# Kernel tuning notes

Hardware: AMD Instinct MI355X
Metric: run time of the kernel (lower is better)

The kernel has to match this reference:

```python
import jax, jax.numpy as jnp
import numpy as np

N = 100000   # total nodes in batched graph
E = 320000   # total edges
B = 128      # number of graphs in batch
D_IN = 128
H = 256
OUT = 10
L = 4        # num_layers - 1 conv layers
EPS = 1e-6


def setup_inputs() -> dict:
    key = jax.random.key(0)
    ks = jax.random.split(key, 8)
    h = jax.random.normal(ks[0], (N, D_IN), dtype=jnp.float32)
    src = jax.random.randint(ks[1], (E,), 0, N)
    dst = jax.random.randint(ks[2], (E,), 0, N)
    batch_ids = jnp.sort(jax.random.randint(ks[3], (N,), 0, B))
    s = 0.05
    W_first = jax.random.normal(ks[4], (D_IN, H), dtype=jnp.float32) * s
    b_first = jnp.zeros((H,), jnp.float32)
    W_rest = jax.random.normal(ks[5], (L - 1, H, H), dtype=jnp.float32) * s
    b_rest = jnp.zeros((L - 1, H), jnp.float32)
    gamma = jnp.ones((L, H), jnp.float32)
    beta = jnp.zeros((L, H), jnp.float32)
    mean_scale = jnp.ones((L, H), jnp.float32)
    W_pred = jax.random.normal(ks[6], (H, OUT), dtype=jnp.float32) * s
    b_pred = jnp.zeros((OUT,), jnp.float32)
    return dict(h=h, src=src, dst=dst, batch_ids=batch_ids,
                W_first=W_first, b_first=b_first, W_rest=W_rest, b_rest=b_rest,
                gamma=gamma, beta=beta, mean_scale=mean_scale,
                W_pred=W_pred, b_pred=b_pred)


def _graph_conv(h, W, b, src, dst, dinv_src, dinv_dst):
    # DGL GraphConv, norm='both': D_dst^{-1/2} A D_src^{-1/2} h W + b
    x = h * dinv_src[:, None]
    m = jax.ops.segment_sum(x[src], dst, num_segments=N)
    m = m * dinv_dst[:, None]
    return m @ W + b


def _graph_norm(h, gamma, beta, ms, batch_ids, counts):
    # GraphNorm: per-graph mean (scaled by learnable mean_scale) and std
    mean = jax.ops.segment_sum(h, batch_ids, num_segments=B) / counts[:, None]
    sub = h - mean[batch_ids] * ms
    var = jax.ops.segment_sum(sub * sub, batch_ids, num_segments=B) / counts[:, None]
    inv_std = jax.lax.rsqrt(var + EPS)
    return gamma * sub * inv_std[batch_ids] + beta


def reference(h, src, dst, batch_ids, W_first, b_first, W_rest, b_rest,
              gamma, beta, mean_scale, W_pred, b_pred):
    ones_e = jnp.ones((E,), h.dtype)
    deg_out = jnp.maximum(jax.ops.segment_sum(ones_e, src, num_segments=N), 1.0)
    deg_in = jnp.maximum(jax.ops.segment_sum(ones_e, dst, num_segments=N), 1.0)
    dinv_src = jax.lax.rsqrt(deg_out)
    dinv_dst = jax.lax.rsqrt(deg_in)
    counts = jnp.maximum(
        jax.ops.segment_sum(jnp.ones((N,), h.dtype), batch_ids, num_segments=B), 1.0)

    for i in range(L):
        x = h
        if i == 0:
            h = _graph_conv(h, W_first, b_first, src, dst, dinv_src, dinv_dst)
        else:
            h = _graph_conv(h, W_rest[i - 1], b_rest[i - 1], src, dst, dinv_src, dinv_dst)
        h = _graph_norm(h, gamma[i], beta[i], mean_scale[i], batch_ids, counts)
        if i != 0:
            h = jax.nn.relu(h) + x
        else:
            h = jax.nn.relu(h)

    pooled = jax.ops.segment_sum(h, batch_ids, num_segments=B)  # [B, H]
    # dropout is identity at eval
    return pooled @ W_pred + b_pred
```

## Files before the change

kernel.cpp:

```cpp
#include <hip/hip_runtime.h>

#define N_NODES 100000
#define N_PAD   100096
#define N_EDGES 320000
#define NB      128
#define DIN     128
#define H       256
#define OUT_DIM 10
#define EPSV    1e-6f
#define SCAN_B  256
#define PSLICES 32

typedef unsigned short bf16_t;
typedef __attribute__((ext_vector_type(8))) short bf16x8;
typedef __attribute__((ext_vector_type(4))) float f32x4;

__device__ __forceinline__ float bf2f(bf16_t u) {
    union { unsigned int i; float f; } x;
    x.i = ((unsigned int)u) << 16;
    return x.f;
}
__device__ __forceinline__ bf16_t f2bf(float f) {
    union { float f; unsigned int i; } x;
    x.f = f;
    unsigned int r = x.i + 0x7fffu + ((x.i >> 16) & 1u);
    return (bf16_t)(r >> 16);
}

__global__ void k_edge_deg(const int* __restrict__ src, const int* __restrict__ dst,
                           int* deg_out, int* deg_in) {
    int e = blockIdx.x * blockDim.x + threadIdx.x;
    if (e < N_EDGES) {
        atomicAdd(&deg_out[src[e]], 1);
        atomicAdd(&deg_in[dst[e]], 1);
    }
}

__global__ void k_dinv(const int* __restrict__ deg_out, const int* __restrict__ deg_in,
                       float* dinv_src, float* dinv_dst) {
    int n = blockIdx.x * blockDim.x + threadIdx.x;
    if (n < N_NODES) {
        dinv_src[n] = rsqrtf((float)max(deg_out[n], 1));
        dinv_dst[n] = rsqrtf((float)max(deg_in[n], 1));
    }
}

__global__ void k_gstart(const int* __restrict__ bid, int* __restrict__ gstart,
                         float* __restrict__ countsf) {
    int b = threadIdx.x;
    if (b <= NB) {
        int lo = 0, hi = N_NODES;
        while (lo < hi) {
            int mid = (lo + hi) >> 1;
            if (bid[mid] < b) lo = mid + 1; else hi = mid;
        }
        gstart[b] = lo;
    }
    __syncthreads();
    if (b < NB) countsf[b] = (float)max(gstart[b + 1] - gstart[b], 1);
}

__global__ void k_scan1(const int* __restrict__ deg, int* incl, int* bsums) {
    __shared__ int s[SCAN_B];
    int i = blockIdx.x * SCAN_B + threadIdx.x;
    int v = (i < N_NODES) ? deg[i] : 0;
    s[threadIdx.x] = v;
    __syncthreads();
    for (int d = 1; d < SCAN_B; d <<= 1) {
        int t = (threadIdx.x >= d) ? s[threadIdx.x - d] : 0;
        __syncthreads();
        s[threadIdx.x] += t;
        __syncthreads();
    }
    if (i < N_NODES) incl[i] = s[threadIdx.x];
    if (threadIdx.x == SCAN_B - 1) bsums[blockIdx.x] = s[threadIdx.x];
}

__global__ void k_scan2(const int* __restrict__ bsums, int* boffs, int nb) {
    __shared__ int s[512];
    int t = threadIdx.x;
    int v = (t < nb) ? bsums[t] : 0;
    s[t] = v;
    __syncthreads();
    for (int d = 1; d < 512; d <<= 1) {
        int x = (t >= d) ? s[t - d] : 0;
        __syncthreads();
        s[t] += x;
        __syncthreads();
    }
    if (t < nb) boffs[t] = s[t] - v;
}

__global__ void k_scan3(const int* __restrict__ deg, const int* __restrict__ incl,
                        const int* __restrict__ boffs, int* row_start, int* cursor) {
    int i = blockIdx.x * blockDim.x + threadIdx.x;
    if (i < N_NODES) {
        int ex = incl[i] - deg[i] + boffs[i / SCAN_B];
        row_start[i] = ex;
        cursor[i]    = ex;
    }
    if (i == 0) row_start[N_NODES] = N_EDGES;
}

__global__ void k_scatter(const int* __restrict__ src, const int* __restrict__ dst,
                          int* cursor, int* csr_src) {
    int e = blockIdx.x * blockDim.x + threadIdx.x;
    if (e < N_EDGES) {
        int slot = atomicAdd(&cursor[dst[e]], 1);
        csr_src[slot] = src[e];
    }
}

__global__ void k_wt_first(const float* __restrict__ W, bf16_t* __restrict__ Wt) {
    int idx = blockIdx.x * 256 + threadIdx.x;
    if (idx >= H * DIN) return;
    int c = idx / DIN, k = idx % DIN;
    Wt[idx] = f2bf(W[k * H + c]);
}
__global__ void k_wt_rest(const float* __restrict__ W, bf16_t* __restrict__ Wt) {
    int idx = blockIdx.x * 256 + threadIdx.x;
    if (idx >= 3 * H * H) return;
    int l = idx / (H * H);
    int rem = idx % (H * H);
    int c = rem / H, k = rem % H;
    Wt[idx] = f2bf(W[(size_t)l * H * H + k * H + c]);
}

__global__ void k_prescale(const float* __restrict__ h, const float* __restrict__ dinv_s,
                           bf16_t* __restrict__ hs) {
    int idx = blockIdx.x * blockDim.x + threadIdx.x;
    if (idx >= N_NODES * (DIN / 4)) return;
    int n = idx >> 5;
    float w = dinv_s[n];
    float4 v = reinterpret_cast<const float4*>(h)[idx];
    ushort4 o;
    o.x = f2bf(v.x * w); o.y = f2bf(v.y * w);
    o.z = f2bf(v.z * w); o.w = f2bf(v.w * w);
    reinterpret_cast<ushort4*>(hs)[idx] = o;
}

template <int NC, bool PS>
__global__ void k_agg(const bf16_t* __restrict__ hx, const float* __restrict__ dinv_s,
                      const float* __restrict__ dinv_d, const int* __restrict__ row_start,
                      const int* __restrict__ csr_src, bf16_t* __restrict__ m) {
    constexpr int VEC = NC / 64;
    int gid  = blockIdx.x * blockDim.x + threadIdx.x;
    int v    = gid >> 6;
    int lane = gid & 63;
    if (v >= N_NODES) return;
    float acc[VEC] = {};
    int s0 = row_start[v], s1 = row_start[v + 1];

    auto body = [&](int ei) {
        int si = csr_src[ei];
        float wv = 1.f;
        if constexpr (!PS) wv = dinv_s[si];
        if constexpr (VEC == 4) {
            ushort4 r = *reinterpret_cast<const ushort4*>(hx + (size_t)si * NC + lane * 4);
            acc[0] += bf2f(r.x) * wv; acc[1] += bf2f(r.y) * wv;
            acc[2] += bf2f(r.z) * wv; acc[3] += bf2f(r.w) * wv;
        } else {
            ushort2 r = *reinterpret_cast<const ushort2*>(hx + (size_t)si * NC + lane * 2);
            acc[0] += bf2f(r.x) * wv; acc[1] += bf2f(r.y) * wv;
        }
    };

    int e = s0;
    for (; e + 3 < s1; e += 4) { body(e); body(e + 1); body(e + 2); body(e + 3); }
    for (; e < s1; ++e) body(e);

    float wd = dinv_d[v];
    if constexpr (VEC == 4) {
        ushort4 o;
        o.x = f2bf(acc[0] * wd); o.y = f2bf(acc[1] * wd);
        o.z = f2bf(acc[2] * wd); o.w = f2bf(acc[3] * wd);
        *reinterpret_cast<ushort4*>(m + (size_t)v * NC + lane * 4) = o;
    } else {
        ushort2 o; o.x = f2bf(acc[0] * wd); o.y = f2bf(acc[1] * wd);
        *reinterpret_cast<ushort2*>(m + (size_t)v * NC + lane * 2) = o;
    }
}

template <int K>
__global__ __launch_bounds__(256) void k_gemm_mfma(const bf16_t* __restrict__ A,
                                                   const bf16_t* __restrict__ Wt,
                                                   const float* __restrict__ bias,
                                                   bf16_t* __restrict__ C) {
    __shared__ bf16_t lds_raw[64 * (H + 8)];
    constexpr int LKA = K + 8;
    bf16_t (*aT)[LKA] = reinterpret_cast<bf16_t (*)[LKA]>(lds_raw);
    bf16_t (*cT)[H + 8] = reinterpret_cast<bf16_t (*)[H + 8]>(lds_raw);

    const int tid  = threadIdx.x;
    const int wave = tid >> 6;
    const int lane = tid & 63;
    const int row0 = blockIdx.x * 64;
    const int col0 = wave * 64;
    const int lr = lane & 15;
    const int lg = lane >> 4;

    {
        const bf16_t* Ag = A + (size_t)row0 * K;
        constexpr int CHUNKS = 64 * K / 8;
        #pragma unroll
        for (int it = 0; it < CHUNKS / 256; ++it) {
            int ci  = it * 256 + tid;
            int row = (ci * 8) / K;
            int col = (ci * 8) % K;
            uint4 v = *reinterpret_cast<const uint4*>(Ag + ci * 8);
            *reinterpret_cast<uint4*>(&aT[row][col]) = v;
        }
    }
    __syncthreads();

    f32x4 acc[4][4] = {};

    const bf16_t* Bb = Wt + (size_t)(col0 + lr) * K + lg * 8;

    #pragma unroll
    for (int ks = 0; ks < K / 32; ++ks) {
        bf16x8 a[4], b[4];
        #pragma unroll
        for (int mt = 0; mt < 4; ++mt)
            a[mt] = *reinterpret_cast<const bf16x8*>(&aT[mt * 16 + lr][ks * 32 + lg * 8]);
        #pragma unroll
        for (int nt = 0; nt < 4; ++nt)
            b[nt] = *reinterpret_cast<const bf16x8*>(Bb + (size_t)nt * 16 * K + ks * 32);
        #pragma unroll
        for (int mt = 0; mt < 4; ++mt)
            #pragma unroll
            for (int nt = 0; nt < 4; ++nt)
                acc[mt][nt] = __builtin_amdgcn_mfma_f32_16x16x32_bf16(a[mt], b[nt], acc[mt][nt], 0, 0, 0);
    }

    __syncthreads();

    #pragma unroll
    for (int nt = 0; nt < 4; ++nt) {
        int c = col0 + nt * 16 + lr;
        float bs = bias[c];
        #pragma unroll
        for (int mt = 0; mt < 4; ++mt) {
            #pragma unroll
            for (int j = 0; j < 4; ++j)
                cT[mt * 16 + lg * 4 + j][c] = f2bf(acc[mt][nt][j] + bs);
        }
    }
    __syncthreads();

    #pragma unroll
    for (int it = 0; it < 8; ++it) {
        int i = it * 256 + tid;
        int r = i >> 5;
        int s = i & 31;
        *reinterpret_cast<uint4*>(C + (size_t)(row0 + r) * H + s * 8) =
            *reinterpret_cast<const uint4*>(&cT[r][s * 8]);
    }
}

__global__ __launch_bounds__(512) void k_stats(const bf16_t* __restrict__ C,
                                               const int* __restrict__ gstart,
                                               float* __restrict__ gsum,
                                               float* __restrict__ gsumsq) {
    __shared__ float red[8][64][9];
    int b   = blockIdx.x;
    int t   = threadIdx.x;
    int grp = t >> 6;
    int ln  = t & 63;
    int n0 = gstart[b], n1 = gstart[b + 1];
    float s[4] = {}, q[4] = {};
    for (int n = n0 + grp; n < n1; n += 8) {
        ushort4 v = *reinterpret_cast<const ushort4*>(C + (size_t)n * H + ln * 4);
        float x0 = bf2f(v.x), x1 = bf2f(v.y), x2 = bf2f(v.z), x3 = bf2f(v.w);
        s[0] += x0; q[0] += x0 * x0;
        s[1] += x1; q[1] += x1 * x1;
        s[2] += x2; q[2] += x2 * x2;
        s[3] += x3; q[3] += x3 * x3;
    }
    #pragma unroll
    for (int j = 0; j < 4; ++j) { red[grp][ln][j] = s[j]; red[grp][ln][4 + j] = q[j]; }
    __syncthreads();
    if (grp == 0) {
        #pragma unroll
        for (int g = 1; g < 8; ++g)
            #pragma unroll
            for (int j = 0; j < 4; ++j) { s[j] += red[g][ln][j]; q[j] += red[g][ln][4 + j]; }
        float4 s4 = { s[0], s[1], s[2], s[3] };
        float4 q4 = { q[0], q[1], q[2], q[3] };
        reinterpret_cast<float4*>(gsum   + (size_t)b * H)[ln] = s4;
        reinterpret_cast<float4*>(gsumsq + (size_t)b * H)[ln] = q4;
    }
}

template <bool RES>
__global__ void k_norm(const bf16_t* __restrict__ y, const bf16_t* __restrict__ resid,
                       const int* __restrict__ bid, const float* __restrict__ gsum,
                       const float* __restrict__ gsumsq, const float* __restrict__ countsf,
                       const float* __restrict__ gamma, const float* __restrict__ beta,
                       const float* __restrict__ msc, bf16_t* __restrict__ outp) {
    int idx = blockIdx.x * blockDim.x + threadIdx.x;
    if (idx >= N_NODES * (H / 4)) return;
    int n  = idx >> 6;
    int f4 = idx & 63;
    int b  = bid[n];
    float rc = 1.0f / countsf[b];
    float4 s4  = reinterpret_cast<const float4*>(gsum)[b * 64 + f4];
    float4 q4  = reinterpret_cast<const float4*>(gsumsq)[b * 64 + f4];
    float4 g4  = reinterpret_cast<const float4*>(gamma)[f4];
    float4 be4 = reinterpret_cast<const float4*>(beta)[f4];
    float4 m4  = reinterpret_cast<const float4*>(msc)[f4];
    ushort4 yv = reinterpret_cast<const ushort4*>(y)[idx];

    auto nrm = [&](float s, float q, float ga, float be, float m, float yy) {
        float mean = s * rc, ex2 = q * rc;
        float mm   = mean * m;
        float var  = ex2 - 2.f * mean * mm + mm * mm;
        float a    = ga * rsqrtf(var + EPSV);
        return fmaxf(yy * a + (be - a * mm), 0.f);
    };
    float o0 = nrm(s4.x, q4.x, g4.x, be4.x, m4.x, bf2f(yv.x));
    float o1 = nrm(s4.y, q4.y, g4.y, be4.y, m4.y, bf2f(yv.y));
    float o2 = nrm(s4.z, q4.z, g4.z, be4.z, m4.z, bf2f(yv.z));
    float o3 = nrm(s4.w, q4.w, g4.w, be4.w, m4.w, bf2f(yv.w));
    if constexpr (RES) {
        ushort4 r = reinterpret_cast<const ushort4*>(resid)[idx];
        o0 += bf2f(r.x); o1 += bf2f(r.y); o2 += bf2f(r.z); o3 += bf2f(r.w);
    }
    ushort4 o;
    o.x = f2bf(o0); o.y = f2bf(o1); o.z = f2bf(o2); o.w = f2bf(o3);
    reinterpret_cast<ushort4*>(outp)[idx] = o;
}

__global__ void k_pool(const bf16_t* __restrict__ hf, const int* __restrict__ gstart,
                       float* pooled) {
    int b = blockIdx.x, sl = blockIdx.y, f = threadIdx.x;
    int n0 = gstart[b], n1 = gstart[b + 1];
    int cnt = n1 - n0;
    int lo = n0 + (int)((long long)cnt * sl / PSLICES);
    int hi = n0 + (int)((long long)cnt * (sl + 1) / PSLICES);
    if (lo >= hi) return;
    float s = 0.f;
    for (int n = lo; n < hi; ++n) s += bf2f(hf[(size_t)n * H + f]);
    atomicAdd(&pooled[b * H + f], s);
}

__global__ void k_pred(const float* __restrict__ pooled, const float* __restrict__ Wp,
                       const float* __restrict__ bp, float* __restrict__ outp) {
    __shared__ float row[H];
    int b = blockIdx.x;
    row[threadIdx.x] = pooled[b * H + threadIdx.x];
    __syncthreads();
    if (threadIdx.x < OUT_DIM) {
        float acc = bp[threadIdx.x];
        for (int f = 0; f < H; ++f) acc += row[f] * Wp[f * OUT_DIM + threadIdx.x];
        outp[b * OUT_DIM + threadIdx.x] = acc;
    }
}

extern "C" void kernel_launch(void* const* d_in, const int* in_sizes, int n_in,
                              void* d_out, int out_size, void* d_ws, size_t ws_size,
                              hipStream_t stream) {
    const float* h_in  = (const float*)d_in[0];
    const int*   src   = (const int*)d_in[1];
    const int*   dst   = (const int*)d_in[2];
    const int*   bid   = (const int*)d_in[3];
    const float* Wf    = (const float*)d_in[4];
    const float* bfv   = (const float*)d_in[5];
    const float* Wr    = (const float*)d_in[6];
    const float* br    = (const float*)d_in[7];
    const float* gamma = (const float*)d_in[8];
    const float* beta  = (const float*)d_in[9];
    const float* ms    = (const float*)d_in[10];
    const float* Wp    = (const float*)d_in[11];
    const float* bp    = (const float*)d_in[12];
    float* outp = (float*)d_out;

    char* w = (char*)d_ws;
    size_t off = 0;
    auto alloc = [&](size_t bytes) -> void* {
        void* p = w + off;
        off = (off + bytes + 255) & ~(size_t)255;
        return p;
    };
    bf16_t* bufA = (bf16_t*)alloc((size_t)N_PAD * H * 2);
    bf16_t* bufB = (bf16_t*)alloc((size_t)N_PAD * H * 2);
    bf16_t* bufC = (bf16_t*)alloc((size_t)N_PAD * H * 2);
    bf16_t* Wt0  = (bf16_t*)alloc((size_t)H * DIN * 2);
    bf16_t* Wt123= (bf16_t*)alloc((size_t)3 * H * H * 2);
    int* deg_out_i = (int*)alloc(N_NODES * 4);
    int* deg_in_i  = (int*)alloc(N_NODES * 4);
    float* dinv_src = (float*)alloc(N_NODES * 4);
    float* dinv_dst = (float*)alloc(N_NODES * 4);
    int* incl_tmp  = (int*)alloc(N_NODES * 4);
    int* bsums     = (int*)alloc(512 * 4);
    int* boffs     = (int*)alloc(512 * 4);
    int* row_start = (int*)alloc((N_NODES + 1) * 4);
    int* cursor    = (int*)alloc(N_NODES * 4);
    int* csr_src   = (int*)alloc(N_EDGES * 4);
    int* gstart    = (int*)alloc((NB + 1) * 4);
    float* countsf = (float*)alloc(NB * 4);
    float* gsum    = (float*)alloc((size_t)NB * H * 4);
    float* gsumsq  = (float*)alloc((size_t)NB * H * 4);
    float* pooled  = (float*)alloc(NB * H * 4);

    if (off > ws_size) return;

    bf16_t* hs = bufB;

    const int nscan = (N_NODES + SCAN_B - 1) / SCAN_B;

    hipMemsetAsync(deg_out_i, 0, N_NODES * 4, stream);
    hipMemsetAsync(deg_in_i, 0, N_NODES * 4, stream);
    hipMemsetAsync(pooled, 0, NB * H * 4, stream);

    k_edge_deg<<<(N_EDGES + 255) / 256, 256, 0, stream>>>(src, dst, deg_out_i, deg_in_i);
    k_gstart<<<1, 256, 0, stream>>>(bid, gstart, countsf);
    k_dinv<<<(N_NODES + 255) / 256, 256, 0, stream>>>(deg_out_i, deg_in_i, dinv_src, dinv_dst);
    k_scan1<<<nscan, SCAN_B, 0, stream>>>(deg_in_i, incl_tmp, bsums);
    k_scan2<<<1, 512, 0, stream>>>(bsums, boffs, nscan);
    k_scan3<<<(N_NODES + 255) / 256, 256, 0, stream>>>(deg_in_i, incl_tmp, boffs, row_start, cursor);
    k_scatter<<<(N_EDGES + 255) / 256, 256, 0, stream>>>(src, dst, cursor, csr_src);
    k_wt_first<<<(H * DIN + 255) / 256, 256, 0, stream>>>(Wf, Wt0);
    k_wt_rest<<<(3 * H * H + 255) / 256, 256, 0, stream>>>(Wr, Wt123);

    const int aggGrid  = (N_NODES + 3) / 4;
    const int normGrid = (N_NODES * (H / 4) + 255) / 256;
    const int gemmGrid = N_PAD / 64;

    k_prescale<<<(N_NODES * (DIN / 4) + 255) / 256, 256, 0, stream>>>(h_in, dinv_src, hs);
    k_agg<DIN, true><<<aggGrid, 256, 0, stream>>>(hs, nullptr, dinv_dst, row_start, csr_src, bufA);
    k_gemm_mfma<DIN><<<gemmGrid, 256, 0, stream>>>(bufA, Wt0, bfv, bufB);
    k_stats<<<NB, 512, 0, stream>>>(bufB, gstart, gsum, gsumsq);
    k_norm<false><<<normGrid, 256, 0, stream>>>(bufB, nullptr, bid, gsum, gsumsq, countsf,
                                                gamma, beta, ms, bufC);

    bf16_t* hx = bufC;
    bf16_t* f1 = bufA;
    bf16_t* f2 = bufB;
    for (int i = 1; i < 4; ++i) {
        k_agg<H, false><<<aggGrid, 256, 0, stream>>>(hx, dinv_src, dinv_dst, row_start, csr_src, f1);
        k_gemm_mfma<H><<<gemmGrid, 256, 0, stream>>>(f1, Wt123 + (size_t)(i - 1) * H * H,
                                                     br + (i - 1) * H, f2);
        k_stats<<<NB, 512, 0, stream>>>(f2, gstart, gsum, gsumsq);
        k_norm<true><<<normGrid, 256, 0, stream>>>(f2, hx, bid, gsum, gsumsq, countsf,
                                                   gamma + i * H, beta + i * H, ms + i * H, f1);
        bf16_t* nh = f1; f1 = hx; hx = nh;
    }

    k_pool<<<dim3(NB, PSLICES), H, 0, stream>>>(hx, gstart, pooled);
    k_pred<<<NB, H, 0, stream>>>(pooled, Wp, bp, outp);
}
```

Before: 671.1 us.

## Fuse per-graph sum/sumsq statistics into GEMM epilogue with partial reduction

```diff
diff --git a/kernel.cpp b/kernel.cpp
--- a/kernel.cpp
+++ b/kernel.cpp
@@ -10,6 +10,7 @@
 #define EPSV    1e-6f
 #define SCAN_B  256
 #define PSLICES 32
+#define NBLK    (N_PAD / 64)
 
 typedef unsigned short bf16_t;
 typedef __attribute__((ext_vector_type(8))) short bf16x8;
@@ -185,8 +186,11 @@
 __global__ __launch_bounds__(256) void k_gemm_mfma(const bf16_t* __restrict__ A,
                                                    const bf16_t* __restrict__ Wt,
                                                    const float* __restrict__ bias,
-                                                   bf16_t* __restrict__ C) {
+                                                   const int* __restrict__ bid,
+                                                   bf16_t* __restrict__ C,
+                                                   float2* __restrict__ part) {
     __shared__ bf16_t lds_raw[64 * (H + 8)];
+    __shared__ int bid_lds[64];
     constexpr int LKA = K + 8;
     bf16_t (*aT)[LKA] = reinterpret_cast<bf16_t (*)[LKA]>(lds_raw);
     bf16_t (*cT)[H + 8] = reinterpret_cast<bf16_t (*)[H + 8]>(lds_raw);
@@ -210,6 +214,10 @@
             uint4 v = *reinterpret_cast<const uint4*>(Ag + ci * 8);
             *reinterpret_cast<uint4*>(&aT[row][col]) = v;
         }
+    }
+    if (tid < 64) {
+        int r = row0 + tid;
+        bid_lds[tid] = (r < N_NODES) ? bid[r] : -1;
     }
     __syncthreads();
 
@@ -256,40 +264,48 @@
         *reinterpret_cast<uint4*>(C + (size_t)(row0 + r) * H + s * 8) =
             *reinterpret_cast<const uint4*>(&cT[r][s * 8]);
     }
-}
-
-__global__ __launch_bounds__(512) void k_stats(const bf16_t* __restrict__ C,
-                                               const int* __restrict__ gstart,
-                                               float* __restrict__ gsum,
-                                               float* __restrict__ gsumsq) {
-    __shared__ float red[8][64][9];
-    int b   = blockIdx.x;
-    int t   = threadIdx.x;
-    int grp = t >> 6;
-    int ln  = t & 63;
+
+    {
+        const int c = tid;
+        float s0 = 0.f, q0 = 0.f, s1 = 0.f, q1 = 0.f, s2 = 0.f, q2 = 0.f;
+        const int g0 = bid_lds[0];
+        for (int r = 0; r < 64; ++r) {
+            int g = bid_lds[r];
+            if (g < 0) break;
+            float v = bf2f(cT[r][c]);
+            int rel = g - g0;
+            if (rel == 0)      { s0 += v; q0 += v * v; }
+            else if (rel == 1) { s1 += v; q1 += v * v; }
+            else if (rel == 2) { s2 += v; q2 += v * v; }
+        }
+        size_t base = (size_t)blockIdx.x * H + c;
+        constexpr size_t PLANE = (size_t)NBLK * H;
+        part[0 * PLANE + base] = make_float2(s0, q0);
+        part[1 * PLANE + base] = make_float2(s1, q1);
+        part[2 * PLANE + base] = make_float2(s2, q2);
+    }
+}
+
+__global__ void k_stats_red(const float2* __restrict__ part, const int* __restrict__ bid,
+                            const int* __restrict__ gstart,
+                            float* __restrict__ gsum, float* __restrict__ gsumsq) {
+    constexpr size_t PLANE = (size_t)NBLK * H;
+    int b = blockIdx.x;
+    int c = threadIdx.x;
     int n0 = gstart[b], n1 = gstart[b + 1];
-    float s[4] = {}, q[4] = {};
-    for (int n = n0 + grp; n < n1; n += 8) {
-        ushort4 v = *reinterpret_cast<const ushort4*>(C + (size_t)n * H + ln * 4);
-        float x0 = bf2f(v.x), x1 = bf2f(v.y), x2 = bf2f(v.z), x3 = bf2f(v.w);
-        s[0] += x0; q[0] += x0 * x0;
-        s[1] += x1; q[1] += x1 * x1;
-        s[2] += x2; q[2] += x2 * x2;
-        s[3] += x3; q[3] += x3 * x3;
-    }
-    #pragma unroll
-    for (int j = 0; j < 4; ++j) { red[grp][ln][j] = s[j]; red[grp][ln][4 + j] = q[j]; }
-    __syncthreads();
-    if (grp == 0) {
-        #pragma unroll
-        for (int g = 1; g < 8; ++g)
-            #pragma unroll
-            for (int j = 0; j < 4; ++j) { s[j] += red[g][ln][j]; q[j] += red[g][ln][4 + j]; }
-        float4 s4 = { s[0], s[1], s[2], s[3] };
-        float4 q4 = { q[0], q[1], q[2], q[3] };
-        reinterpret_cast<float4*>(gsum   + (size_t)b * H)[ln] = s4;
-        reinterpret_cast<float4*>(gsumsq + (size_t)b * H)[ln] = q4;
-    }
+    float s = 0.f, q = 0.f;
+    if (n1 > n0) {
+        int blo = n0 >> 6, bhi = (n1 - 1) >> 6;
+        for (int blk = blo; blk <= bhi; ++blk) {
+            int rel = b - bid[blk << 6];
+            if (rel >= 0 && rel < 3) {
+                float2 v = part[(size_t)rel * PLANE + (size_t)blk * H + c];
+                s += v.x; q += v.y;
+            }
+        }
+    }
+    gsum[b * H + c]   = s;
+    gsumsq[b * H + c] = q;
 }
 
 template <bool RES>
@@ -401,6 +417,7 @@
     float* countsf = (float*)alloc(NB * 4);
     float* gsum    = (float*)alloc((size_t)NB * H * 4);
     float* gsumsq  = (float*)alloc((size_t)NB * H * 4);
+    float2* part   = (float2*)alloc((size_t)3 * NBLK * H * 8);
     float* pooled  = (float*)alloc(NB * H * 4);
 
     if (off > ws_size) return;
@@ -425,12 +442,12 @@
 
     const int aggGrid  = (N_NODES + 3) / 4;
     const int normGrid = (N_NODES * (H / 4) + 255) / 256;
-    const int gemmGrid = N_PAD / 64;
+    const int gemmGrid = NBLK;
 
     k_prescale<<<(N_NODES * (DIN / 4) + 255) / 256, 256, 0, stream>>>(h_in, dinv_src, hs);
     k_agg<DIN, true><<<aggGrid, 256, 0, stream>>>(hs, nullptr, dinv_dst, row_start, csr_src, bufA);
-    k_gemm_mfma<DIN><<<gemmGrid, 256, 0, stream>>>(bufA, Wt0, bfv, bufB);
-    k_stats<<<NB, 512, 0, stream>>>(bufB, gstart, gsum, gsumsq);
+    k_gemm_mfma<DIN><<<gemmGrid, 256, 0, stream>>>(bufA, Wt0, bfv, bid, bufB, part);
+    k_stats_red<<<NB, H, 0, stream>>>(part, bid, gstart, gsum, gsumsq);
     k_norm<false><<<normGrid, 256, 0, stream>>>(bufB, nullptr, bid, gsum, gsumsq, countsf,
                                                 gamma, beta, ms, bufC);
 
@@ -440,8 +457,8 @@
     for (int i = 1; i < 4; ++i) {
         k_agg<H, false><<<aggGrid, 256, 0, stream>>>(hx, dinv_src, dinv_dst, row_start, csr_src, f1);
         k_gemm_mfma<H><<<gemmGrid, 256, 0, stream>>>(f1, Wt123 + (size_t)(i - 1) * H * H,
-                                                     br + (i - 1) * H, f2);
-        k_stats<<<NB, 512, 0, stream>>>(f2, gstart, gsum, gsumsq);
+                                                     br + (i - 1) * H, bid, f2, part);
+        k_stats_red<<<NB, H, 0, stream>>>(part, bid, gstart, gsum, gsumsq);
         k_norm<true><<<normGrid, 256, 0, stream>>>(f2, hx, bid, gsum, gsumsq, countsf,
                                                    gamma + i * H, beta + i * H, ms + i * H, f1);
         bf16_t* nh = f1; f1 = hx; hx = nh;
```

New measurement: 656.4 us. -2.2%, faster.
